# Performance work log

Measured on AMD Instinct MI355X. Metric: run time of the kernel, lower is better.

Reference implementation:

```python
import jax, jax.numpy as jnp
import numpy as np

HEADS = 4
NEG_SLOPE = 0.2  # DGL GATConv default leaky_relu slope


def _gat_conv(h, src, dst, W, al, ar, resW, b, heads, out_feats, num_nodes):
    """DGL GATConv semantics with prefix-shape support.
    h: [N, *prefix, in]; returns [N, *prefix, heads, out_feats].
    """
    prefix = h.shape[1:-1]
    z = jnp.einsum('...i,ij->...j', h, W).reshape(h.shape[0], *prefix, heads, out_feats)
    # per-node attention halves: [N, *prefix, heads, 1]
    el = jnp.sum(z * al, axis=-1, keepdims=True)
    er = jnp.sum(z * ar, axis=-1, keepdims=True)
    # per-edge logits: [E, *prefix, heads, 1]
    e = jax.nn.leaky_relu(el[src] + er[dst], NEG_SLOPE)
    # edge softmax over incoming edges of each dst node (stable)
    emax = jax.ops.segment_max(e, dst, num_segments=num_nodes)
    emax = jax.lax.stop_gradient(jnp.where(jnp.isfinite(emax), emax, 0.0))
    ex = jnp.exp(e - emax[dst])
    denom = jax.ops.segment_sum(ex, dst, num_segments=num_nodes)
    a = ex / jnp.where(denom == 0, 1.0, denom)[dst]
    # weighted scatter-aggregate of messages
    rst = jax.ops.segment_sum(z[src] * a, dst, num_segments=num_nodes)
    # residual projection + bias + relu activation
    res = jnp.einsum('...i,ij->...j', h, resW).reshape(h.shape[0], *prefix, heads, out_feats)
    return jax.nn.relu(rst + res + b.reshape(heads, out_feats))


def setup_inputs() -> dict:
    key = jax.random.key(0)
    ks = jax.random.split(key, 16)
    N, E, IN, HID, OUT2, CLS = 8192, 65536, 256, 512, 32, 40
    def w(k, shape, fan_in):
        return jax.random.normal(k, shape, dtype=jnp.float32) * (1.0 / np.sqrt(fan_in))
    return {
        'features': jax.random.normal(ks[0], (N, IN), dtype=jnp.float32),
        'src': jax.random.randint(ks[1], (E,), 0, N, dtype=jnp.int32),
        'dst': jax.random.randint(ks[2], (E,), 0, N, dtype=jnp.int32),
        # layer 1: in=256 -> heads=4, out=512
        'W1': w(ks[3], (IN, HEADS * HID), IN),
        'al1': w(ks[4], (HEADS, HID), HID),
        'ar1': w(ks[5], (HEADS, HID), HID),
        'resW1': w(ks[6], (IN, HEADS * HID), IN),
        'b1': jnp.zeros((HEADS * HID,), dtype=jnp.float32),
        # layer 2: in=512 -> heads=4, out=32 (applied per prefix head dim)
        'W2': w(ks[7], (HID, HEADS * OUT2), HID),
        'al2': w(ks[8], (HEADS, OUT2), OUT2),
        'ar2': w(ks[9], (HEADS, OUT2), OUT2),
        'resW2': w(ks[10], (HID, HEADS * OUT2), HID),
        'b2': jnp.zeros((HEADS * OUT2,), dtype=jnp.float32),
        # final linear: 32*4^2 = 512 -> 40
        'Wout': w(ks[11], (OUT2 * HEADS * HEADS, CLS), OUT2 * HEADS * HEADS),
        'bout': jnp.zeros((CLS,), dtype=jnp.float32),
    }


def reference(features, src, dst, W1, al1, ar1, resW1, b1, W2, al2, ar2, resW2, b2, Wout, bout):
    N = features.shape[0]
    # dropout is identity at inference
    h1 = _gat_conv(features, src, dst, W1, al1, ar1, resW1, b1, HEADS, 512, N)  # [N,4,512]
    h2 = _gat_conv(h1, src, dst, W2, al2, ar2, resW2, b2, HEADS, 32, N)        # [N,4,4,32]
    h = h2.reshape(N, -1)  # [N,512]
    return h @ Wout + bout
```

## Files before the change

### kernel.cpp

```cpp
#include <hip/hip_runtime.h>
#include <cmath>

constexpr int IN_F  = 256;

typedef short bf16x8 __attribute__((ext_vector_type(8)));
typedef short short4v __attribute__((ext_vector_type(4)));
typedef float f32x4 __attribute__((ext_vector_type(4)));

__device__ __forceinline__ short f2bf(float f) {
    unsigned u = __float_as_uint(f);
    unsigned r = (u + 0x7FFFu + ((u >> 16) & 1)) >> 16;
    return (short)r;
}
__device__ __forceinline__ float b2f(short s) {
    return __uint_as_float(((unsigned)(unsigned short)s) << 16);
}

__device__ __forceinline__ int xcd_logical_id()
{
    int nx = gridDim.x, ny = gridDim.y, nz = gridDim.z;
    int flat = blockIdx.x + nx * (blockIdx.y + ny * blockIdx.z);
    int nwg = nx * ny * nz;
    if (nwg & 7) return flat;
    int chunk = nwg >> 3;
    return (flat & 7) * chunk + (flat >> 3);
}

__device__ __forceinline__ void cvt_t_body(
    const float* __restrict__ W, short* __restrict__ Wt, int K, int N,
    int ldwt, int koff, int bk, int bn, int tx, int ty)
{
    __shared__ float tile[32][33];
    for (int i = ty; i < 32; i += 8) {
        int gn = bn + tx;
        tile[i][tx] = (gn < N) ? W[(size_t)(bk + i) * N + gn] : 0.f;
    }
    __syncthreads();
    for (int i = ty; i < 32; i += 8)
        Wt[(size_t)(bn + i) * ldwt + koff + bk + tx] = f2bf(tile[tx][i]);
}

__global__ __launch_bounds__(256) void prep_all(
    const float* __restrict__ W1, const float* __restrict__ al1, const float* __restrict__ ar1,
    const float* __restrict__ resW1, const float* __restrict__ resW2,
    const float* __restrict__ W2, const float* __restrict__ Wout, const float* __restrict__ b2,
    short* __restrict__ Wcomb, short* __restrict__ W2comb, short* __restrict__ Wtout,
    float* __restrict__ wal1, float* __restrict__ war1,
    float* __restrict__ bias2c, int* __restrict__ zero_base)
{
    int bid = blockIdx.x;
    int t   = threadIdx.x;
    if (bid < 256) {
        int wid  = (bid * 256 + t) >> 6;
        int lane = t & 63;
        int k = wid >> 2, h = wid & 3;
        const float* wr  = W1  + (size_t)k * 2048 + h * 512;
        const float* alp = al1 + h * 512;
        const float* arp = ar1 + h * 512;
        float sl = 0.f, sr = 0.f;
        for (int j = lane; j < 512; j += 64) {
            float wv = wr[j];
            sl = fmaf(wv, alp[j], sl);
            sr = fmaf(wv, arp[j], sr);
        }
#pragma unroll
        for (int o = 32; o; o >>= 1) { sl += __shfl_down(sl, o); sr += __shfl_down(sr, o); }
        if (lane == 0) { wal1[wid] = sl; war1[wid] = sr; }
    } else if (bid < 1280) {
        int id = bid - 256;
        int bx = id & 63, by = (id >> 6) & 7, bz = id >> 9;
        const float* W = bz ? resW1 : W1;
        cvt_t_body(W, Wcomb, 256, 2048, 512, bz ? 256 : 0,
                   by * 32, bx * 32, t & 31, t >> 5);
    } else if (bid < 1472) {
        int id = bid - 1280;
        int bx = id & 3, by = (id >> 2) & 15, bz = id >> 6;
        const float* W; short* Wt; int N;
        if (bz == 0)      { W = W2;    Wt = W2comb;             N = 128; }
        else if (bz == 1) { W = resW2; Wt = W2comb + 128 * 512; N = 128; }
        else              { W = Wout;  Wt = Wtout;              N = 40;  }
        cvt_t_body(W, Wt, 512, N, 512, 0, by * 32, bx * 32, t & 31, t >> 5);
    } else if (bid == 1472) {
        bias2c[t] = (t < 128) ? 0.f : b2[t - 128];
    } else {
        int b = bid - 1473;
        int4 z; z.x = 0; z.y = 0; z.z = 0; z.w = 0;
        ((int4*)zero_base)[(size_t)b * 256 + t] = z;
    }
}

__global__ __launch_bounds__(256) void l1_front(
    const float* __restrict__ feat, const float4* __restrict__ wal, const float4* __restrict__ war,
    short* __restrict__ featb, float* __restrict__ el, float* __restrict__ er,
    const int* __restrict__ dst, int* __restrict__ deg, int E, int nfeat)
{
    if ((int)blockIdx.x >= nfeat) {
        int e = (blockIdx.x - nfeat) * 256 + threadIdx.x;
        if (e < E) atomicAdd(&deg[dst[e]], 1);
        return;
    }
    int row  = blockIdx.x * 4 + (threadIdx.x >> 6);
    int lane = threadIdx.x & 63;
    float4 v = ((const float4*)feat)[(size_t)row * 64 + lane];
    short4v o;
    o[0] = f2bf(v.x); o[1] = f2bf(v.y); o[2] = f2bf(v.z); o[3] = f2bf(v.w);
    *(short4v*)(featb + (size_t)row * 256 + lane * 4) = o;

    float fj[4] = { v.x, v.y, v.z, v.w };
    int k = lane * 4;
    float sl[4] = {}, sr[4] = {};
#pragma unroll
    for (int j = 0; j < 4; j++) {
        float4 wl = wal[k + j], wr = war[k + j];
        sl[0] = fmaf(fj[j], wl.x, sl[0]); sl[1] = fmaf(fj[j], wl.y, sl[1]);
        sl[2] = fmaf(fj[j], wl.z, sl[2]); sl[3] = fmaf(fj[j], wl.w, sl[3]);
        sr[0] = fmaf(fj[j], wr.x, sr[0]); sr[1] = fmaf(fj[j], wr.y, sr[1]);
        sr[2] = fmaf(fj[j], wr.z, sr[2]); sr[3] = fmaf(fj[j], wr.w, sr[3]);
    }
#pragma unroll
    for (int o2 = 32; o2; o2 >>= 1) {
#pragma unroll
        for (int h = 0; h < 4; h++) { sl[h] += __shfl_down(sl[h], o2); sr[h] += __shfl_down(sr[h], o2); }
    }
    if (lane == 0) {
#pragma unroll
        for (int h = 0; h < 4; h++) { el[row * 4 + h] = sl[h]; er[row * 4 + h] = sr[h]; }
    }
}

__global__ __launch_bounds__(256) void gemm_bf16(
    const short* __restrict__ A, const short* __restrict__ Bt,
    const float* __restrict__ bias, void* __restrict__ C,
    int M, int N, int K, int ldc, int nmax, int out_bf16,
    float* __restrict__ el2, float* __restrict__ er2,
    const float* __restrict__ al2, const float* __restrict__ ar2, int do_el)
{
    __shared__ short sA[2][128 * 32];
    __shared__ short sB[2][128 * 32];
    const int tid  = threadIdx.x;
    const int wave = tid >> 6, lane = tid & 63;
    const int wm = wave >> 1, wn = wave & 1;
    int lid = xcd_logical_id();
    const int bx = lid % gridDim.x, by = lid / gridDim.x;
    const int m0 = by * 128, n0 = bx * 128;

    const int srow = tid >> 2;
    const int scol = (tid & 3) * 8;
    const int fr = lane & 15;
    const int fq = lane >> 4;

    f32x4 acc[4][4] = {};

    for (int k0 = 0; k0 < K; k0 += 64) {
#pragma unroll
        for (int hh = 0; hh < 2; hh++) {
            int kc = k0 + hh * 32 + scol;
            const short* ga0 = A  + (size_t)(m0 + srow) * K + kc;
            const short* ga1 = A  + (size_t)(m0 + 64 + srow) * K + kc;
            const short* gb0 = Bt + (size_t)(n0 + srow) * K + kc;
            const short* gb1 = Bt + (size_t)(n0 + 64 + srow) * K + kc;
            __builtin_amdgcn_global_load_lds((const __attribute__((address_space(1))) void*)ga0,
                (__attribute__((address_space(3))) void*)(sA[hh] + wave * 512), 16, 0, 0);
            __builtin_amdgcn_global_load_lds((const __attribute__((address_space(1))) void*)ga1,
                (__attribute__((address_space(3))) void*)(sA[hh] + 2048 + wave * 512), 16, 0, 0);
            __builtin_amdgcn_global_load_lds((const __attribute__((address_space(1))) void*)gb0,
                (__attribute__((address_space(3))) void*)(sB[hh] + wave * 512), 16, 0, 0);
            __builtin_amdgcn_global_load_lds((const __attribute__((address_space(1))) void*)gb1,
                (__attribute__((address_space(3))) void*)(sB[hh] + 2048 + wave * 512), 16, 0, 0);
        }
        __syncthreads();

#pragma unroll
        for (int hh = 0; hh < 2; hh++) {
            bf16x8 af[4], bfr[4];
#pragma unroll
            for (int m = 0; m < 4; m++)
                af[m] = *(const bf16x8*)(sA[hh] + (wm * 64 + m * 16 + fr) * 32 + fq * 8);
#pragma unroll
            for (int n = 0; n < 4; n++)
                bfr[n] = *(const bf16x8*)(sB[hh] + (wn * 64 + n * 16 + fr) * 32 + fq * 8);
#pragma unroll
            for (int m = 0; m < 4; m++)
#pragma unroll
                for (int n = 0; n < 4; n++)
                    acc[m][n] = __builtin_amdgcn_mfma_f32_16x16x32_bf16(af[m], bfr[n], acc[m][n], 0, 0, 0);
        }
        __syncthreads();
    }

    if (do_el && bx == 0) {
        float cal[4], car[4];
#pragma unroll
        for (int n = 0; n < 4; n++) {
            cal[n] = al2[wn * 64 + n * 16 + fr];
            car[n] = ar2[wn * 64 + n * 16 + fr];
        }
#pragma unroll
        for (int m = 0; m < 4; m++) {
#pragma unroll
            for (int j = 0; j < 4; j++) {
                float ell = acc[m][0][j] * cal[0] + acc[m][1][j] * cal[1];
                float elh = acc[m][2][j] * cal[2] + acc[m][3][j] * cal[3];
                float erl = acc[m][0][j] * car[0] + acc[m][1][j] * car[1];
                float erh = acc[m][2][j] * car[2] + acc[m][3][j] * car[3];
#pragma unroll
                for (int o = 1; o < 16; o <<= 1) {
                    ell += __shfl_xor(ell, o);
                    elh += __shfl_xor(elh, o);
                    erl += __shfl_xor(erl, o);
                    erh += __shfl_xor(erh, o);
                }
                if (fr == 0) {
                    int R = m0 + wm * 64 + m * 16 + fq * 4 + j;
                    el2[R * 4 + wn * 2]     = ell;
                    el2[R * 4 + wn * 2 + 1] = elh;
                    er2[R * 4 + wn * 2]     = erl;
                    er2[R * 4 + wn * 2 + 1] = erh;
                }
            }
        }
    }

#pragma unroll
    for (int n = 0; n < 4; n++) {
        int gcol = n0 + wn * 64 + n * 16 + fr;
        if (gcol >= nmax) continue;
        float bv = bias ? bias[gcol] : 0.f;
#pragma unroll
        for (int m = 0; m < 4; m++) {
#pragma unroll
            for (int j = 0; j < 4; j++) {
                int grow = m0 + wm * 64 + m * 16 + fq * 4 + j;
                float v = acc[m][n][j] + bv;
                if (out_bf16) ((short*)C)[(size_t)grow * ldc + gcol] = f2bf(v);
                else          ((float*)C)[(size_t)grow * ldc + gcol] = v;
            }
        }
    }
}

__global__ __launch_bounds__(256) void gemm_h1(
    const short* __restrict__ Acomb, const short* __restrict__ featb,
    const short* __restrict__ Wcomb, const float* __restrict__ b1, short* __restrict__ h1b)
{
    __shared__ short sA[2][128 * 32];
    __shared__ short sB[2][128 * 32];
    const int tid  = threadIdx.x;
    const int wave = tid >> 6, lane = tid & 63;
    const int wm = wave >> 1, wn = wave & 1;
    int lid = xcd_logical_id();
    const int bx = lid & 3;
    const int by = (lid >> 2) % gridDim.y;
    const int h  = lid / (gridDim.y * 4);
    const int m0 = by * 128, n0 = bx * 128;
    const short* Bt = Wcomb + (size_t)(h * 512) * 512;

    const int srow = tid >> 2;
    const int scol = (tid & 3) * 8;
    const int fr = lane & 15;
    const int fq = lane >> 4;

    f32x4 acc[4][4] = {};

    for (int k0 = 0; k0 < 512; k0 += 64) {
        const int res_half = (k0 >= 256);
#pragma unroll
        for (int hh = 0; hh < 2; hh++) {
            int kc = k0 + hh * 32 + scol;
            const short* ga0;
            const short* ga1;
            if (!res_half) {
                ga0 = Acomb + ((size_t)(m0 + srow) * 4 + h) * 256 + kc;
                ga1 = Acomb + ((size_t)(m0 + 64 + srow) * 4 + h) * 256 + kc;
            } else {
                ga0 = featb + (size_t)(m0 + srow) * 256 + (kc - 256);
                ga1 = featb + (size_t)(m0 + 64 + srow) * 256 + (kc - 256);
            }
            const short* gb0 = Bt + (size_t)(n0 + srow) * 512 + kc;
            const short* gb1 = Bt + (size_t)(n0 + 64 + srow) * 512 + kc;
            __builtin_amdgcn_global_load_lds((const __attribute__((address_space(1))) void*)ga0,
                (__attribute__((address_space(3))) void*)(sA[hh] + wave * 512), 16, 0, 0);
            __builtin_amdgcn_global_load_lds((const __attribute__((address_space(1))) void*)ga1,
                (__attribute__((address_space(3))) void*)(sA[hh] + 2048 + wave * 512), 16, 0, 0);
            __builtin_amdgcn_global_load_lds((const __attribute__((address_space(1))) void*)gb0,
                (__attribute__((address_space(3))) void*)(sB[hh] + wave * 512), 16, 0, 0);
            __builtin_amdgcn_global_load_lds((const __attribute__((address_space(1))) void*)gb1,
                (__attribute__((address_space(3))) void*)(sB[hh] + 2048 + wave * 512), 16, 0, 0);
        }
        __syncthreads();

#pragma unroll
        for (int hh = 0; hh < 2; hh++) {
            bf16x8 af[4], bfr[4];
#pragma unroll
            for (int m = 0; m < 4; m++)
                af[m] = *(const bf16x8*)(sA[hh] + (wm * 64 + m * 16 + fr) * 32 + fq * 8);
#pragma unroll
            for (int n = 0; n < 4; n++)
                bfr[n] = *(const bf16x8*)(sB[hh] + (wn * 64 + n * 16 + fr) * 32 + fq * 8);
#pragma unroll
            for (int m = 0; m < 4; m++)
#pragma unroll
                for (int n = 0; n < 4; n++)
                    acc[m][n] = __builtin_amdgcn_mfma_f32_16x16x32_bf16(af[m], bfr[n], acc[m][n], 0, 0, 0);
        }
        __syncthreads();
    }

#pragma unroll
    for (int n = 0; n < 4; n++) {
        int gcol = h * 512 + n0 + wn * 64 + n * 16 + fr;
        float bv = b1[gcol];
#pragma unroll
        for (int m = 0; m < 4; m++) {
#pragma unroll
            for (int j = 0; j < 4; j++) {
                int grow = m0 + wm * 64 + m * 16 + fq * 4 + j;
                float v = acc[m][n][j] + bv;
                h1b[(size_t)grow * 2048 + gcol] = f2bf(v > 0.f ? v : 0.f);
            }
        }
    }
}

__global__ __launch_bounds__(1024) void scan_excl(const int* __restrict__ deg,
                                                  int* __restrict__ off, int N)
{
    __shared__ int part[1024];
    int t = threadIdx.x;
    int chunk = N >> 10;
    int base = t * chunk;
    int local[16];
    int s = 0;
    for (int i = 0; i < chunk; i++) { local[i] = s; s += deg[base + i]; }
    part[t] = s;
    __syncthreads();
    for (int o = 1; o < 1024; o <<= 1) {
        int v = (t >= o) ? part[t - o] : 0;
        __syncthreads();
        part[t] += v;
        __syncthreads();
    }
    int pre = (t == 0) ? 0 : part[t - 1];
    for (int i = 0; i < chunk; i++) off[base + i] = pre + local[i];
    if (t == 1023) off[N] = pre + s;
}

__global__ void scatter_kernel(const int* __restrict__ dst, const int* __restrict__ off,
                               int* __restrict__ cur, int* __restrict__ eid, int E)
{
    int e = blockIdx.x * blockDim.x + threadIdx.x;
    if (e < E) {
        int d = dst[e];
        int p = off[d] + atomicAdd(&cur[d], 1);
        eid[p] = e;
    }
}

__global__ __launch_bounds__(256) void aggregate_feat_sm(
    const int* __restrict__ off, const int* __restrict__ eid, const int* __restrict__ src,
    const float* __restrict__ el, const float* __restrict__ er,
    const short* __restrict__ featb, short* __restrict__ Acomb)
{
    int wv = threadIdx.x >> 6, lane = threadIdx.x & 63;
    int n = blockIdx.x * 4 + wv;
    int k4 = lane * 4;
    float4 erv = ((const float4*)er)[n];
    float acc[4][4] = {};
    float accd[4] = {};
    int beg = off[n], end = off[n + 1];
    for (int j = beg; j < end; ++j) {
        int e = eid[j];
        int s = src[e];
        float4 elv = ((const float4*)el)[s];
        float a0 = elv.x + erv.x, a1 = elv.y + erv.y, a2 = elv.z + erv.z, a3 = elv.w + erv.w;
        a0 = __expf(a0 > 0.f ? a0 : 0.2f * a0);
        a1 = __expf(a1 > 0.f ? a1 : 0.2f * a1);
        a2 = __expf(a2 > 0.f ? a2 : 0.2f * a2);
        a3 = __expf(a3 > 0.f ? a3 : 0.2f * a3);
        accd[0] += a0; accd[1] += a1; accd[2] += a2; accd[3] += a3;
        short4v fv = *(const short4v*)(featb + (size_t)s * 256 + k4);
        float f0 = b2f(fv[0]), f1 = b2f(fv[1]), f2 = b2f(fv[2]), f3 = b2f(fv[3]);
        acc[0][0] = fmaf(a0, f0, acc[0][0]); acc[0][1] = fmaf(a0, f1, acc[0][1]);
        acc[0][2] = fmaf(a0, f2, acc[0][2]); acc[0][3] = fmaf(a0, f3, acc[0][3]);
        acc[1][0] = fmaf(a1, f0, acc[1][0]); acc[1][1] = fmaf(a1, f1, acc[1][1]);
        acc[1][2] = fmaf(a1, f2, acc[1][2]); acc[1][3] = fmaf(a1, f3, acc[1][3]);
        acc[2][0] = fmaf(a2, f0, acc[2][0]); acc[2][1] = fmaf(a2, f1, acc[2][1]);
        acc[2][2] = fmaf(a2, f2, acc[2][2]); acc[2][3] = fmaf(a2, f3, acc[2][3]);
        acc[3][0] = fmaf(a3, f0, acc[3][0]); acc[3][1] = fmaf(a3, f1, acc[3][1]);
        acc[3][2] = fmaf(a3, f2, acc[3][2]); acc[3][3] = fmaf(a3, f3, acc[3][3]);
    }
    float inv[4];
#pragma unroll
    for (int h = 0; h < 4; h++) inv[h] = 1.f / (accd[h] == 0.f ? 1.f : accd[h]);
#pragma unroll
    for (int h = 0; h < 4; h++) {
        short4v o;
#pragma unroll
        for (int kk = 0; kk < 4; kk++) o[kk] = f2bf(acc[h][kk] * inv[h]);
        *(short4v*)(Acomb + ((size_t)n * 4 + h) * 256 + k4) = o;
    }
}

__global__ __launch_bounds__(256) void aggregate2_sm(
    const int* __restrict__ off, const int* __restrict__ eid, const int* __restrict__ src,
    const float* __restrict__ el, const float* __restrict__ er,
    const short* __restrict__ z2res, short* __restrict__ h2)
{
    int n = blockIdx.x, t = threadIdx.x;
    int c = t >> 4;
    int p = t >> 6;
    int rem = (2 * t) & 127;
    float erv = er[n * 16 + c];
    float r0 = 0.f, r1 = 0.f, dn = 0.f;
    int beg = off[n], end = off[n + 1];
    for (int j = beg; j < end; ++j) {
        int e = eid[j];
        int s = src[e];
        float lv = el[s * 16 + c] + erv;
        float a = __expf(lv > 0.f ? lv : 0.2f * lv);
        dn += a;
        unsigned zv = *(const unsigned*)(z2res + ((size_t)s * 4 + p) * 256 + rem);
        r0 = fmaf(a, b2f((short)(zv & 0xFFFFu)), r0);
        r1 = fmaf(a, b2f((short)(zv >> 16)), r1);
    }
    if (dn == 0.f) dn = 1.f;
    float inv = 1.f / dn;
    unsigned rv = *(const unsigned*)(z2res + ((size_t)n * 4 + p) * 256 + 128 + rem);
    float v0 = r0 * inv + b2f((short)(rv & 0xFFFFu));
    float v1 = r1 * inv + b2f((short)(rv >> 16));
    v0 = v0 > 0.f ? v0 : 0.f;
    v1 = v1 > 0.f ? v1 : 0.f;
    unsigned o = ((unsigned)(unsigned short)f2bf(v1) << 16) | (unsigned)(unsigned short)f2bf(v0);
    *(unsigned*)(h2 + (size_t)n * 512 + t * 2) = o;
}

extern "C" void kernel_launch(void* const* d_in, const int* in_sizes, int n_in,
                              void* d_out, int out_size, void* d_ws, size_t ws_size,
                              hipStream_t stream)
{
    const float* feat  = (const float*)d_in[0];
    const int*   src   = (const int*)d_in[1];
    const int*   dst   = (const int*)d_in[2];
    const float* W1    = (const float*)d_in[3];
    const float* al1   = (const float*)d_in[4];
    const float* ar1   = (const float*)d_in[5];
    const float* resW1 = (const float*)d_in[6];
    const float* b1    = (const float*)d_in[7];
    const float* W2    = (const float*)d_in[8];
    const float* al2   = (const float*)d_in[9];
    const float* ar2   = (const float*)d_in[10];
    const float* resW2 = (const float*)d_in[11];
    const float* b2    = (const float*)d_in[12];
    const float* Wout  = (const float*)d_in[13];
    const float* bout  = (const float*)d_in[14];
    const int N = in_sizes[0] / IN_F;
    const int E = in_sizes[1];

    char* w = (char*)d_ws;
    auto alloc = [&](size_t bytes) -> char* {
        char* p = w;
        w += (bytes + 255) & ~(size_t)255;
        return p;
    };
    short*    Acomb   = (short*)alloc((size_t)N * 4 * 256 * 2);
    short*    h1b     = (short*)alloc((size_t)N * 2048 * 2);
    short*    featb   = (short*)alloc((size_t)N * 256 * 2);
    short*    Wcomb   = (short*)alloc((size_t)2048 * 512 * 2);
    short*    W2comb  = (short*)alloc((size_t)256 * 512 * 2);
    short*    Wtout   = (short*)alloc((size_t)128 * 512 * 2);
    float*    bias2c  = (float*)alloc((size_t)256 * 4);
    float*    wal1    = (float*)alloc((size_t)256 * 4 * 4);
    float*    war1    = (float*)alloc((size_t)256 * 4 * 4);
    float*    el1     = (float*)alloc((size_t)N * 4 * 4);
    float*    er1     = (float*)alloc((size_t)N * 4 * 4);
    int*      deg     = (int*)alloc((size_t)N * 4);
    int*      cur     = (int*)alloc((size_t)N * 4);
    int*      off     = (int*)alloc((size_t)(N + 1) * 4);
    int*      eid     = (int*)alloc((size_t)E * 4);
    short*    z2res   = (short*)alloc((size_t)N * 4 * 256 * 2);
    short*    h2b     = (short*)alloc((size_t)N * 512 * 2);
    float*    el2     = (float*)alloc((size_t)N * 16 * 4);
    float*    er2     = (float*)alloc((size_t)N * 16 * 4);

    dim3 blk(256);

    prep_all<<<dim3(1489), blk, 0, stream>>>(W1, al1, ar1, resW1, resW2, W2, Wout, b2,
                                             Wcomb, W2comb, Wtout,
                                             wal1, war1, bias2c, deg);

    l1_front<<<dim3(N / 4 + E / 256), blk, 0, stream>>>(feat, (const float4*)wal1, (const float4*)war1,
                                                        featb, el1, er1, dst, deg, E, N / 4);
    scan_excl<<<dim3(1), dim3(1024), 0, stream>>>(deg, off, N);
    scatter_kernel<<<dim3((E + 255) / 256), blk, 0, stream>>>(dst, off, cur, eid, E);

    aggregate_feat_sm<<<dim3(N / 4), blk, 0, stream>>>(off, eid, src, el1, er1, featb, Acomb);
    gemm_h1<<<dim3(4, N / 128, 4), blk, 0, stream>>>(Acomb, featb, Wcomb, b1, h1b);

    gemm_bf16<<<dim3(2, (N * 4) / 128), blk, 0, stream>>>(h1b, W2comb, bias2c, z2res,
                                                          N * 4, 256, 512, 256, 256, 1,
                                                          el2, er2, al2, ar2, 1);
    aggregate2_sm<<<dim3(N), blk, 0, stream>>>(off, eid, src, el2, er2, z2res, h2b);

    gemm_bf16<<<dim3(1, N / 128), blk, 0, stream>>>(h2b, Wtout, bout, (float*)d_out,
                                                    N, 128, 512, 40, 40, 0,
                                                    nullptr, nullptr, nullptr, nullptr, 0);
}
```

Measured before the change: 143.7 us.

## Fuse layer-2 aggregation with final output linear projection

Merges the layer-2 edge aggregation kernel with the final 512->40 linear layer. Each wavefront now handles one node and loads 8 bf16 features per lane, so every edge gather uses wider 16-byte loads. The fused kernel keeps the relu'd h2 row in registers and takes dot products against an LDS copy of Wtout, finishing with a wave shuffle reduction. This drops the h2 intermediate write and read and one kernel launch. In exchange, every block reloads the 40KB weight into LDS, the final projection becomes scalar FMAs with 40 serial shuffle reductions instead of an MFMA GEMM, and the 40KB of LDS per block may lower occupancy.

```diff
diff --git a/kernel.cpp b/kernel.cpp
--- a/kernel.cpp
+++ b/kernel.cpp
@@ -402,17 +402,24 @@
     }
 }
 
-__global__ __launch_bounds__(256) void aggregate2_sm(
+__global__ __launch_bounds__(256) void aggregate2_out(
     const int* __restrict__ off, const int* __restrict__ eid, const int* __restrict__ src,
     const float* __restrict__ el, const float* __restrict__ er,
-    const short* __restrict__ z2res, short* __restrict__ h2)
-{
-    int n = blockIdx.x, t = threadIdx.x;
-    int c = t >> 4;
-    int p = t >> 6;
-    int rem = (2 * t) & 127;
+    const short* __restrict__ z2res, const short* __restrict__ Wtout,
+    const float* __restrict__ bout, float* __restrict__ out)
+{
+    __shared__ short sW[40 * 512];
+    for (int i = threadIdx.x; i < 40 * 512 / 8; i += 256)
+        *(bf16x8*)(sW + (size_t)i * 8) = *(const bf16x8*)(Wtout + (size_t)i * 8);
+
+    int wv = threadIdx.x >> 6, lane = threadIdx.x & 63;
+    int n = blockIdx.x * 4 + wv;
+    int p = lane >> 4;
+    int colin = (lane & 15) * 8;
+    int c = p * 4 + (colin >> 5);
     float erv = er[n * 16 + c];
-    float r0 = 0.f, r1 = 0.f, dn = 0.f;
+    float r[8] = {};
+    float dn = 0.f;
     int beg = off[n], end = off[n + 1];
     for (int j = beg; j < end; ++j) {
         int e = eid[j];
@@ -420,19 +427,30 @@
         float lv = el[s * 16 + c] + erv;
         float a = __expf(lv > 0.f ? lv : 0.2f * lv);
         dn += a;
-        unsigned zv = *(const unsigned*)(z2res + ((size_t)s * 4 + p) * 256 + rem);
-        r0 = fmaf(a, b2f((short)(zv & 0xFFFFu)), r0);
-        r1 = fmaf(a, b2f((short)(zv >> 16)), r1);
+        bf16x8 zv = *(const bf16x8*)(z2res + ((size_t)s * 4 + p) * 256 + colin);
+#pragma unroll
+        for (int i = 0; i < 8; ++i) r[i] = fmaf(a, b2f(zv[i]), r[i]);
     }
     if (dn == 0.f) dn = 1.f;
     float inv = 1.f / dn;
-    unsigned rv = *(const unsigned*)(z2res + ((size_t)n * 4 + p) * 256 + 128 + rem);
-    float v0 = r0 * inv + b2f((short)(rv & 0xFFFFu));
-    float v1 = r1 * inv + b2f((short)(rv >> 16));
-    v0 = v0 > 0.f ? v0 : 0.f;
-    v1 = v1 > 0.f ? v1 : 0.f;
-    unsigned o = ((unsigned)(unsigned short)f2bf(v1) << 16) | (unsigned)(unsigned short)f2bf(v0);
-    *(unsigned*)(h2 + (size_t)n * 512 + t * 2) = o;
+    bf16x8 rv = *(const bf16x8*)(z2res + ((size_t)n * 4 + p) * 256 + 128 + colin);
+    float h2v[8];
+#pragma unroll
+    for (int i = 0; i < 8; ++i) {
+        float v = r[i] * inv + b2f(rv[i]);
+        h2v[i] = v > 0.f ? v : 0.f;
+    }
+    __syncthreads();
+
+    for (int c2 = 0; c2 < 40; c2++) {
+        bf16x8 w8 = *(const bf16x8*)(sW + c2 * 512 + lane * 8);
+        float s = 0.f;
+#pragma unroll
+        for (int i = 0; i < 8; ++i) s = fmaf(h2v[i], b2f(w8[i]), s);
+#pragma unroll
+        for (int o = 32; o; o >>= 1) s += __shfl_down(s, o);
+        if (lane == 0) out[(size_t)n * 40 + c2] = s + bout[c2];
+    }
 }
 
 extern "C" void kernel_launch(void* const* d_in, const int* in_sizes, int n_in,
@@ -479,7 +497,6 @@
     int*      off     = (int*)alloc((size_t)(N + 1) * 4);
     int*      eid     = (int*)alloc((size_t)E * 4);
     short*    z2res   = (short*)alloc((size_t)N * 4 * 256 * 2);
-    short*    h2b     = (short*)alloc((size_t)N * 512 * 2);
     float*    el2     = (float*)alloc((size_t)N * 16 * 4);
     float*    er2     = (float*)alloc((size_t)N * 16 * 4);
 
@@ -500,9 +517,7 @@
     gemm_bf16<<<dim3(2, (N * 4) / 128), blk, 0, stream>>>(h1b, W2comb, bias2c, z2res,
                                                           N * 4, 256, 512, 256, 256, 1,
                                                           el2, er2, al2, ar2, 1);
-    aggregate2_sm<<<dim3(N), blk, 0, stream>>>(off, eid, src, el2, er2, z2res, h2b);
-
-    gemm_bf16<<<dim3(1, N / 128), blk, 0, stream>>>(h2b, Wtout, bout, (float*)d_out,
-                                                    N, 128, 512, 40, 40, 0,
-                                                    nullptr, nullptr, nullptr, nullptr, 0);
-}
+
+    aggregate2_out<<<dim3(N / 4), blk, 0, stream>>>(off, eid, src, el2, er2, z2res,
+                                                    Wtout, bout, (float*)d_out);
+}
```

Result: slower. 154.8 us (+7.7%).
